# Optimization experiments

Hardware: AMD Instinct MI355X
Metric: run time of the kernel (lower is better)

The kernel has to match this reference:

```python
import jax, jax.numpy as jnp
import numpy as np

B, F, D, H, E, K = 4, 2048, 1024, 2048, 8, 2  # batch, frames, dim, expert hidden, n_experts, top_k


def setup_inputs() -> dict:
    key = jax.random.key(0)
    ks = jax.random.split(key, 9)
    sc = lambda k, shape, fan_in: (jax.random.normal(k, shape, jnp.float32) * (fan_in ** -0.5))
    return {
        "x": jax.random.normal(ks[0], (B, F, D), jnp.float32),
        # router: Linear(D,D) -> SiLU -> Linear(D,E)
        "rw1": sc(ks[1], (D, D), D),
        "rb1": jnp.zeros((D,), jnp.float32),
        "rw2": sc(ks[2], (D, E), D),
        "rb2": jnp.zeros((E,), jnp.float32),
        # experts: E x (Linear(D,H) -> SiLU -> Linear(H,D))
        "ew1": sc(ks[3], (E, D, H), D),
        "eb1": jnp.zeros((E, H), jnp.float32),
        "ew2": sc(ks[4], (E, H, D), H),
        "eb2": jnp.zeros((E, D), jnp.float32),
    }


def reference(x, rw1, rb1, rw2, rb2, ew1, eb1, ew2, eb2):
    b, f, d = x.shape
    t = x.reshape(b * f, d)                                   # [T, D]
    # router (eval mode: no topk noise)
    logits = jax.nn.silu(t @ rw1 + rb1) @ rw2 + rb2            # [T, E]
    vals, idx = jax.lax.top_k(logits, K)                       # [T, K]
    rows = jnp.arange(t.shape[0])[:, None]
    masked = jnp.full_like(logits, -jnp.inf).at[rows, idx].set(vals)
    w = jax.nn.softmax(masked, axis=1)                         # [T, E], nonzero only on top-k
    # dense per-expert FFN, then weighted combine (residual: y starts as x)
    eh = jax.nn.silu(jnp.einsum('td,edh->teh', t, ew1) + eb1[None])   # [T, E, H]
    eo = jnp.einsum('teh,ehd->ted', eh, ew2) + eb2[None]              # [T, E, D]
    y = t + jnp.einsum('te,ted->td', w, eo)
    return y.reshape(b, f, d)
```

## Files before the change

### kernel.cpp

```cpp
#include <hip/hip_runtime.h>
#include <hip/hip_bf16.h>
#include <cstdint>
#include <cstddef>

#define T_TOK 8192
#define DDIM  1024
#define HDIM  2048
#define NEXP  8
#define TOPK  2
#define KAUG  (3 * DDIM)

typedef short bf16x8 __attribute__((ext_vector_type(8)));
typedef float f32x4  __attribute__((ext_vector_type(4)));

__device__ __forceinline__ unsigned short f2bf(float f) {
  union { float f; unsigned u; } v; v.f = f;
  unsigned r = v.u + 0x7FFFu + ((v.u >> 16) & 1u);
  return (unsigned short)(r >> 16);
}
__device__ __forceinline__ float bf2f(unsigned short h) {
  union { unsigned u; float f; } v; v.u = ((unsigned)h) << 16;
  return v.f;
}
__device__ __forceinline__ float silu_fast(float v) {
  return v / (1.0f + __expf(-v));
}
__device__ __forceinline__ float silu_precise(float v) {
  return v / (1.0f + expf(-v));
}

__device__ __forceinline__ void gload16(const unsigned short* g, unsigned short* l) {
  __builtin_amdgcn_global_load_lds(
      (const __attribute__((address_space(1))) unsigned int*)g,
      (__attribute__((address_space(3))) unsigned int*)l,
      16, 0, 0);
}

__global__ void split_x_kernel(const float* __restrict__ in,
                               unsigned short* __restrict__ xaug, int n4) {
  int i = blockIdx.x * blockDim.x + threadIdx.x;
  if (i >= n4) return;
  float4 v = ((const float4*)in)[i];
  int t = i / (DDIM / 4);
  int kc = (i % (DDIM / 4)) * 4;
  float f[4] = {v.x, v.y, v.z, v.w};
  ushort4 hi, lo;
  unsigned short h[4], l[4];
#pragma unroll
  for (int j = 0; j < 4; j++) {
    h[j] = f2bf(f[j]);
    l[j] = f2bf(f[j] - bf2f(h[j]));
  }
  hi.x = h[0]; hi.y = h[1]; hi.z = h[2]; hi.w = h[3];
  lo.x = l[0]; lo.y = l[1]; lo.z = l[2]; lo.w = l[3];
  *(ushort4*)&xaug[(size_t)t * KAUG + kc] = hi;
  *(ushort4*)&xaug[(size_t)t * KAUG + DDIM + kc] = hi;
  *(ushort4*)&xaug[(size_t)t * KAUG + 2 * DDIM + kc] = lo;
}

__global__ __launch_bounds__(256) void split_w_kernel(
    const float* __restrict__ in, unsigned short* __restrict__ waug) {
  __shared__ float tile[32][33];
  int c0 = blockIdx.x * 32, r0 = blockIdx.y * 32;
  int tx = threadIdx.x & 31, ty = threadIdx.x >> 5;
#pragma unroll
  for (int i = 0; i < 32; i += 8)
    tile[ty + i][tx] = in[(size_t)(r0 + ty + i) * DDIM + (c0 + tx)];
  __syncthreads();
#pragma unroll
  for (int i = 0; i < 32; i += 8) {
    float v = tile[tx][ty + i];
    unsigned short h = f2bf(v);
    unsigned short l = f2bf(v - bf2f(h));
    int n = c0 + ty + i, k = r0 + tx;
    waug[(size_t)n * KAUG + k] = h;
    waug[(size_t)n * KAUG + DDIM + k] = l;
    waug[(size_t)n * KAUG + 2 * DDIM + k] = h;
  }
}

__global__ __launch_bounds__(256) void transpose_conv_kernel(
    const float* __restrict__ in, unsigned short* __restrict__ out, int R, int C) {
  __shared__ float tile[32][33];
  const int z = blockIdx.z;
  const float* src = in + (size_t)z * R * C;
  unsigned short* dst = out + (size_t)z * R * C;
  int c0 = blockIdx.x * 32, r0 = blockIdx.y * 32;
  int tx = threadIdx.x & 31, ty = threadIdx.x >> 5;
#pragma unroll
  for (int i = 0; i < 32; i += 8)
    tile[ty + i][tx] = src[(size_t)(r0 + ty + i) * C + (c0 + tx)];
  __syncthreads();
#pragma unroll
  for (int i = 0; i < 32; i += 8)
    dst[(size_t)(c0 + ty + i) * R + (r0 + tx)] = f2bf(tile[tx][ty + i]);
}

__global__ void zero_small_kernel(int* __restrict__ counts, int* __restrict__ cursors) {
  int i = threadIdx.x;
  if (i < NEXP) { counts[i] = 0; cursors[i] = 0; }
}

template <int EPI>
__global__ __launch_bounds__(256) void gemm_mfma(
    const unsigned short* __restrict__ Abase,
    const unsigned short* __restrict__ Btbase,
    const float* __restrict__ bias,
    float* __restrict__ outF,
    unsigned short* __restrict__ outBf,
    const int* __restrict__ toks,
    const int* __restrict__ offs, const int* __restrict__ cnts,
    int N, int KD, int Astride, int numE, int nTiles, int mCap) {
  const int id = blockIdx.x;
  const int e = id % numE;
  const int r = id / numE;
  const int n0 = (r % nTiles) * 128;
  const int mb = r / nTiles;

  int ne = T_TOK, off = 0;
  if (EPI != 0) { ne = cnts[e]; off = offs[e]; }

  const unsigned short* Bt = Btbase + (size_t)e * N * KD;
  const unsigned short* A = (EPI == 2) ? (Abase + (size_t)off * Astride) : Abase;

  __shared__ unsigned short As[2][128][32];
  __shared__ unsigned short Bs[2][128][32];

  const int tid  = threadIdx.x;
  const int lane = tid & 63, wid = tid >> 6;
  const int wm = wid >> 1, wn = wid & 1;
  const int quad = lane >> 4, l16 = lane & 15;

  const int rowS0 = tid >> 2;
  const int kc0 = (tid & 3) * 8;

  const size_t brow0 = (size_t)(n0 + rowS0) * KD;
  const size_t brow1 = brow0 + (size_t)64 * KD;
  const int nIter = KD / 32;
  const int mStride = mCap * 128;

  for (int m0 = mb * 128; m0 < ne; m0 += mStride) {
    size_t arow0, arow1;
    if (EPI == 1) {
      int p0 = m0 + rowS0, p1 = m0 + rowS0 + 64;
      int t0 = (p0 < ne) ? toks[off + p0] : 0;
      int t1 = (p1 < ne) ? toks[off + p1] : 0;
      arow0 = (size_t)t0 * Astride;
      arow1 = (size_t)t1 * Astride;
    } else if (EPI == 2) {
      arow0 = (size_t)min(m0 + rowS0, ne - 1) * Astride;
      arow1 = (size_t)min(m0 + rowS0 + 64, ne - 1) * Astride;
    } else {
      arow0 = (size_t)(m0 + rowS0) * Astride;
      arow1 = arow0 + (size_t)64 * Astride;
    }

    f32x4 zf = {0.f, 0.f, 0.f, 0.f};
    f32x4 acc[4][4];
#pragma unroll
    for (int mi = 0; mi < 4; mi++)
#pragma unroll
      for (int ni = 0; ni < 4; ni++) acc[mi][ni] = zf;

    {
      unsigned short* a0 = &As[0][0][0] + wid * 512;
      unsigned short* b0 = &Bs[0][0][0] + wid * 512;
      gload16(A + arow0 + kc0, a0);
      gload16(A + arow1 + kc0, a0 + 2048);
      gload16(Bt + brow0 + kc0, b0);
      gload16(Bt + brow1 + kc0, b0 + 2048);
    }

    for (int k = 0; k < nIter; k++) {
      const int cur = k & 1;
      if (k + 1 < nIter) {
        const int nk = (k + 1) * 32;
        unsigned short* a0 = &As[cur ^ 1][0][0] + wid * 512;
        unsigned short* b0 = &Bs[cur ^ 1][0][0] + wid * 512;
        gload16(A + arow0 + nk + kc0, a0);
        gload16(A + arow1 + nk + kc0, a0 + 2048);
        gload16(Bt + brow0 + nk + kc0, b0);
        gload16(Bt + brow1 + nk + kc0, b0 + 2048);
        __builtin_amdgcn_s_waitcnt(0x0F74);
      } else {
        __builtin_amdgcn_s_waitcnt(0x0F70);
      }
      __builtin_amdgcn_s_barrier();
      bf16x8 af[4], bfr[4];
#pragma unroll
      for (int mi = 0; mi < 4; mi++)
        af[mi] = *(const bf16x8*)&As[cur][wm * 64 + mi * 16 + l16][quad * 8];
#pragma unroll
      for (int ni = 0; ni < 4; ni++)
        bfr[ni] = *(const bf16x8*)&Bs[cur][wn * 64 + ni * 16 + l16][quad * 8];
#pragma unroll
      for (int mi = 0; mi < 4; mi++)
#pragma unroll
        for (int ni = 0; ni < 4; ni++)
          acc[mi][ni] = __builtin_amdgcn_mfma_f32_16x16x32_bf16(
              af[mi], bfr[ni], acc[mi][ni], 0, 0, 0);
      __builtin_amdgcn_s_barrier();
    }

#pragma unroll
    for (int mi = 0; mi < 4; mi++) {
      const int prow_base = wm * 64 + mi * 16 + quad * 4;
#pragma unroll
      for (int rr = 0; rr < 4; rr++) {
        const int p = m0 + prow_base + rr;
        if (EPI != 0 && p >= ne) continue;
#pragma unroll
        for (int ni = 0; ni < 4; ni++) {
          const int col = n0 + wn * 64 + ni * 16 + l16;
          float v = acc[mi][ni][rr] + bias[(size_t)e * N + col];
          if (EPI == 0) {
            outF[(size_t)p * N + col] = silu_precise(v);
          } else if (EPI == 1) {
            outBf[(size_t)(off + p) * N + col] = f2bf(silu_fast(v));
          } else {
            outBf[(size_t)(off + p) * N + col] = f2bf(v);
          }
        }
      }
    }
  }
}

__global__ __launch_bounds__(256) void router2_kernel(
    const float* __restrict__ rh, const float* __restrict__ rw2,
    const float* __restrict__ rb2, float* __restrict__ logits) {
  int t = blockIdx.x * 4 + (threadIdx.x >> 6);
  int lane = threadIdx.x & 63;
  const float* row = rh + (size_t)t * DDIM;
  float acc[NEXP];
#pragma unroll
  for (int e = 0; e < NEXP; e++) acc[e] = 0.f;
  for (int k = lane; k < DDIM; k += 64) {
    float v = row[k];
    const float* w = rw2 + (size_t)k * NEXP;
#pragma unroll
    for (int e = 0; e < NEXP; e++) acc[e] += v * w[e];
  }
#pragma unroll
  for (int e = 0; e < NEXP; e++) {
#pragma unroll
    for (int off = 32; off > 0; off >>= 1) acc[e] += __shfl_xor(acc[e], off, 64);
  }
#pragma unroll
  for (int e = 0; e < NEXP; e++)
    if (lane == e) logits[(size_t)t * NEXP + e] = acc[e] + rb2[e];
}

__global__ void topk_kernel(const float* __restrict__ logits,
                            int* __restrict__ idx2, float* __restrict__ w2arr,
                            int* __restrict__ counts) {
  int t = blockIdx.x * blockDim.x + threadIdx.x;
  if (t >= T_TOK) return;
  float l[NEXP];
#pragma unroll
  for (int e = 0; e < NEXP; e++) l[e] = logits[(size_t)t * NEXP + e];
  int i1 = 0; float v1 = l[0];
#pragma unroll
  for (int e = 1; e < NEXP; e++)
    if (l[e] > v1) { v1 = l[e]; i1 = e; }
  int i2 = -1; float v2 = -3.4e38f;
#pragma unroll
  for (int e = 0; e < NEXP; e++)
    if (e != i1 && l[e] > v2) { v2 = l[e]; i2 = e; }
  float ex = expf(v2 - v1);
  float wa = 1.f / (1.f + ex);
  float wb = ex / (1.f + ex);
  idx2[t * 2] = i1; idx2[t * 2 + 1] = i2;
  w2arr[t * 2] = wa; w2arr[t * 2 + 1] = wb;
  atomicAdd(&counts[i1], 1);
  atomicAdd(&counts[i2], 1);
}

__global__ void prefix_kernel(const int* __restrict__ counts, int* __restrict__ offs) {
  if (threadIdx.x == 0 && blockIdx.x == 0) {
    int s = 0;
    for (int e = 0; e < NEXP; e++) { offs[e] = s; s += counts[e]; }
  }
}

__global__ void scatter_kernel(const int* __restrict__ idx2,
                               const int* __restrict__ offs, int* __restrict__ cursors,
                               int* __restrict__ toks, int* __restrict__ posArr) {
  int t = blockIdx.x * blockDim.x + threadIdx.x;
  if (t >= T_TOK) return;
#pragma unroll
  for (int j = 0; j < TOPK; j++) {
    int e = idx2[t * 2 + j];
    int pos = atomicAdd(&cursors[e], 1);
    int s = offs[e] + pos;
    toks[s] = t;
    posArr[t * 2 + j] = s;
  }
}

__global__ __launch_bounds__(256) void combine_kernel(
    const float* __restrict__ x, const unsigned short* __restrict__ eo,
    const int* __restrict__ posArr, const float* __restrict__ w2arr,
    float* __restrict__ y) {
  const int t = blockIdx.x;
  const int d = threadIdx.x * 4;
  const int s0 = posArr[t * 2], s1 = posArr[t * 2 + 1];
  const float w0 = w2arr[t * 2], w1 = w2arr[t * 2 + 1];
  float4 xv = *(const float4*)&x[(size_t)t * DDIM + d];
  ushort4 a = *(const ushort4*)&eo[(size_t)s0 * DDIM + d];
  ushort4 b = *(const ushort4*)&eo[(size_t)s1 * DDIM + d];
  float4 o;
  o.x = xv.x + w0 * bf2f(a.x) + w1 * bf2f(b.x);
  o.y = xv.y + w0 * bf2f(a.y) + w1 * bf2f(b.y);
  o.z = xv.z + w0 * bf2f(a.z) + w1 * bf2f(b.z);
  o.w = xv.w + w0 * bf2f(a.w) + w1 * bf2f(b.w);
  *(float4*)&y[(size_t)t * DDIM + d] = o;
}

extern "C" void kernel_launch(void* const* d_in, const int* in_sizes, int n_in,
                              void* d_out, int out_size, void* d_ws, size_t ws_size,
                              hipStream_t stream) {
  (void)in_sizes; (void)n_in; (void)out_size; (void)ws_size;
  const float* x   = (const float*)d_in[0];
  const float* rw1 = (const float*)d_in[1];
  const float* rb1 = (const float*)d_in[2];
  const float* rw2 = (const float*)d_in[3];
  const float* rb2 = (const float*)d_in[4];
  const float* ew1 = (const float*)d_in[5];
  const float* eb1 = (const float*)d_in[6];
  const float* ew2 = (const float*)d_in[7];
  const float* eb2 = (const float*)d_in[8];
  float* y = (float*)d_out;

  char* ws = (char*)d_ws;
  size_t o = 0;
  auto alloc = [&](size_t bytes) {
    size_t r = o;
    o += (bytes + 255) & ~(size_t)255;
    return r;
  };
  unsigned short* xaug  = (unsigned short*)(ws + alloc((size_t)T_TOK * KAUG * 2));
  unsigned short* waug  = (unsigned short*)(ws + alloc((size_t)DDIM * KAUG * 2));
  unsigned short* ew1t  = (unsigned short*)(ws + alloc((size_t)NEXP * HDIM * DDIM * 2));
  unsigned short* ew2t  = (unsigned short*)(ws + alloc((size_t)NEXP * DDIM * HDIM * 2));
  float*          rh    = (float*)(ws + alloc((size_t)T_TOK * DDIM * 4));
  float*          logits= (float*)(ws + alloc((size_t)T_TOK * NEXP * 4));
  int*            idx2  = (int*)(ws + alloc((size_t)T_TOK * 2 * 4));
  float*          w2    = (float*)(ws + alloc((size_t)T_TOK * 2 * 4));
  int*            toks  = (int*)(ws + alloc((size_t)T_TOK * TOPK * 4));
  int*            posArr= (int*)(ws + alloc((size_t)T_TOK * TOPK * 4));
  int*            counts= (int*)(ws + alloc(256));
  int*            cursors=(int*)(ws + alloc(256));
  int*            offs  = (int*)(ws + alloc(256));
  unsigned short* ehb   = (unsigned short*)(ws + alloc((size_t)T_TOK * TOPK * HDIM * 2));
  unsigned short* eo    = (unsigned short*)(ws + alloc((size_t)T_TOK * TOPK * DDIM * 2));

  zero_small_kernel<<<1, 64, 0, stream>>>(counts, cursors);

  const int n4 = T_TOK * DDIM / 4;
  split_x_kernel<<<(n4 + 255) / 256, 256, 0, stream>>>(x, xaug, n4);
  split_w_kernel<<<dim3(DDIM / 32, DDIM / 32), 256, 0, stream>>>(rw1, waug);
  transpose_conv_kernel<<<dim3(HDIM / 32, DDIM / 32, NEXP), 256, 0, stream>>>(ew1, ew1t, DDIM, HDIM);
  transpose_conv_kernel<<<dim3(DDIM / 32, HDIM / 32, NEXP), 256, 0, stream>>>(ew2, ew2t, HDIM, DDIM);

  gemm_mfma<0><<<512, 256, 0, stream>>>(
      xaug, waug, rb1, rh, nullptr, nullptr, nullptr, nullptr,
      DDIM, KAUG, KAUG, 1, 8, 64);
  router2_kernel<<<T_TOK / 4, 256, 0, stream>>>(rh, rw2, rb2, logits);
  topk_kernel<<<T_TOK / 256, 256, 0, stream>>>(logits, idx2, w2, counts);
  prefix_kernel<<<1, 64, 0, stream>>>(counts, offs);
  scatter_kernel<<<T_TOK / 256, 256, 0, stream>>>(idx2, offs, cursors, toks, posArr);

  gemm_mfma<1><<<8 * 16 * 16, 256, 0, stream>>>(
      xaug, ew1t, eb1, nullptr, ehb, toks, offs, counts,
      HDIM, DDIM, KAUG, NEXP, 16, 16);
  gemm_mfma<2><<<8 * 8 * 32, 256, 0, stream>>>(
      ehb, ew2t, eb2, nullptr, eo, nullptr, offs, counts,
      DDIM, HDIM, HDIM, NEXP, 8, 32);
  combine_kernel<<<T_TOK, 256, 0, stream>>>(x, eo, posArr, w2, y);
}
```

Baseline: 806.4 us.

## Rewrite MFMA GEMM with 256-row tiles, 512 threads, swizzled LDS and split prefetch

Replaces the 128x128, 256-thread GEMM with a templated kernel that uses 256xBNT tiles, 8 waves and 64-wide K steps. Operands are staged in swizzled dynamic LDS of up to 128KB. The A and B prefetches for the next step are interleaved between two MFMA half-steps, with s_setprio raised around the MFMA blocks. The aim is more operand reuse per LDS load, fewer bank conflicts and better overlap of global loads with MFMA for the router and both expert GEMMs. The cost is much larger LDS and register use per block, which can cut occupancy, and coarser tiles that may waste work on ragged expert counts.

```diff
diff --git a/kernel.cpp b/kernel.cpp
--- a/kernel.cpp
+++ b/kernel.cpp
@@ -101,8 +101,8 @@
   if (i < NEXP) { counts[i] = 0; cursors[i] = 0; }
 }
 
-template <int EPI>
-__global__ __launch_bounds__(256) void gemm_mfma(
+template <int EPI, int BNT>
+__global__ __launch_bounds__(512, 2) void gemm_mfma2(
     const unsigned short* __restrict__ Abase,
     const unsigned short* __restrict__ Btbase,
     const float* __restrict__ bias,
@@ -111,10 +111,15 @@
     const int* __restrict__ toks,
     const int* __restrict__ offs, const int* __restrict__ cnts,
     int N, int KD, int Astride, int numE, int nTiles, int mCap) {
+  constexpr int NI = BNT / 64;
+  constexpr int RB = BNT / 64;
+  constexpr int BB = BNT * 128;
+  extern __shared__ char sm[];
+
   const int id = blockIdx.x;
   const int e = id % numE;
   const int r = id / numE;
-  const int n0 = (r % nTiles) * 128;
+  const int n0 = (r % nTiles) * BNT;
   const int mb = r / nTiles;
 
   int ne = T_TOK, off = 0;
@@ -123,96 +128,129 @@
   const unsigned short* Bt = Btbase + (size_t)e * N * KD;
   const unsigned short* A = (EPI == 2) ? (Abase + (size_t)off * Astride) : Abase;
 
-  __shared__ unsigned short As[2][128][32];
-  __shared__ unsigned short Bs[2][128][32];
-
-  const int tid  = threadIdx.x;
+  const int tid = threadIdx.x;
   const int lane = tid & 63, wid = tid >> 6;
-  const int wm = wid >> 1, wn = wid & 1;
-  const int quad = lane >> 4, l16 = lane & 15;
-
-  const int rowS0 = tid >> 2;
-  const int kc0 = (tid & 3) * 8;
-
-  const size_t brow0 = (size_t)(n0 + rowS0) * KD;
-  const size_t brow1 = brow0 + (size_t)64 * KD;
-  const int nIter = KD / 32;
-  const int mStride = mCap * 128;
-
-  for (int m0 = mb * 128; m0 < ne; m0 += mStride) {
-    size_t arow0, arow1;
-    if (EPI == 1) {
-      int p0 = m0 + rowS0, p1 = m0 + rowS0 + 64;
-      int t0 = (p0 < ne) ? toks[off + p0] : 0;
-      int t1 = (p1 < ne) ? toks[off + p1] : 0;
-      arow0 = (size_t)t0 * Astride;
-      arow1 = (size_t)t1 * Astride;
-    } else if (EPI == 2) {
-      arow0 = (size_t)min(m0 + rowS0, ne - 1) * Astride;
-      arow1 = (size_t)min(m0 + rowS0 + 64, ne - 1) * Astride;
-    } else {
-      arow0 = (size_t)(m0 + rowS0) * Astride;
-      arow1 = arow0 + (size_t)64 * Astride;
+  const int l16 = lane & 15, quad = lane >> 4;
+  const int wm = wid >> 2, wn = wid & 3;
+
+  const int rStage = tid >> 3;
+  const int cS8 = ((tid & 7) ^ (rStage & 7)) * 8;
+  const int ldsW = wid << 10;
+
+  const int NT = KD / 64;
+  const int mStride = mCap * 256;
+
+  const int sw = l16 & 7;
+  const int cOff0 = (quad ^ sw) << 4;
+  const int cOff1 = ((quad + 4) ^ sw) << 4;
+  const int aRowB = (wm * 128 + l16) << 7;
+  const int bRowB = (wn * (NI * 16) + l16) << 7;
+
+  const unsigned short* bPtr[RB];
+#pragma unroll
+  for (int p = 0; p < RB; p++)
+    bPtr[p] = Bt + (size_t)(n0 + p * 64 + rStage) * KD + cS8;
+
+  for (int m0 = mb * 256; m0 < ne; m0 += mStride) {
+    const unsigned short* aPtr[4];
+#pragma unroll
+    for (int p = 0; p < 4; p++) {
+      int row = m0 + p * 64 + rStage;
+      int idx;
+      if (EPI == 1) idx = toks[off + min(row, ne - 1)];
+      else if (EPI == 2) idx = min(row, ne - 1);
+      else idx = row;
+      aPtr[p] = A + (size_t)idx * Astride + cS8;
     }
 
-    f32x4 zf = {0.f, 0.f, 0.f, 0.f};
-    f32x4 acc[4][4];
-#pragma unroll
-    for (int mi = 0; mi < 4; mi++)
-#pragma unroll
-      for (int ni = 0; ni < 4; ni++) acc[mi][ni] = zf;
-
-    {
-      unsigned short* a0 = &As[0][0][0] + wid * 512;
-      unsigned short* b0 = &Bs[0][0][0] + wid * 512;
-      gload16(A + arow0 + kc0, a0);
-      gload16(A + arow1 + kc0, a0 + 2048);
-      gload16(Bt + brow0 + kc0, b0);
-      gload16(Bt + brow1 + kc0, b0 + 2048);
+    f32x4 acc[8][NI];
+    const f32x4 zf = {0.f, 0.f, 0.f, 0.f};
+#pragma unroll
+    for (int mi = 0; mi < 8; mi++)
+#pragma unroll
+      for (int ni = 0; ni < NI; ni++) acc[mi][ni] = zf;
+
+#pragma unroll
+    for (int p = 0; p < 4; p++)
+      gload16(aPtr[p], (unsigned short*)(sm + p * 8192 + ldsW));
+#pragma unroll
+    for (int p = 0; p < RB; p++)
+      gload16(bPtr[p], (unsigned short*)(sm + 65536 + p * 8192 + ldsW));
+    __builtin_amdgcn_s_waitcnt(0x0F70);
+    __builtin_amdgcn_s_barrier();
+    __builtin_amdgcn_sched_barrier(0);
+
+    int cur = 0;
+    for (int t = 0; t < NT; ++t) {
+      const int nxt = cur ^ 1;
+      const bool pf = (t + 1) < NT;
+      const int kb = (t + 1) * 64;
+      const char* cbA = sm + cur * 32768;
+      const char* cbB = sm + 65536 + cur * BB;
+
+      if (pf) {
+#pragma unroll
+        for (int p = 0; p < 4; p++)
+          gload16(aPtr[p] + kb, (unsigned short*)(sm + nxt * 32768 + p * 8192 + ldsW));
+      }
+      bf16x8 av[8], bv[NI];
+#pragma unroll
+      for (int mi = 0; mi < 8; mi++)
+        av[mi] = *(const bf16x8*)(cbA + aRowB + (mi << 11) + cOff0);
+#pragma unroll
+      for (int ni = 0; ni < NI; ni++)
+        bv[ni] = *(const bf16x8*)(cbB + bRowB + (ni << 11) + cOff0);
+      __builtin_amdgcn_s_barrier();
+      __builtin_amdgcn_s_setprio(1);
+#pragma unroll
+      for (int mi = 0; mi < 8; mi++)
+#pragma unroll
+        for (int ni = 0; ni < NI; ni++)
+          acc[mi][ni] = __builtin_amdgcn_mfma_f32_16x16x32_bf16(
+              av[mi], bv[ni], acc[mi][ni], 0, 0, 0);
+      __builtin_amdgcn_s_setprio(0);
+
+      if (pf) {
+#pragma unroll
+        for (int p = 0; p < RB; p++)
+          gload16(bPtr[p] + kb,
+                  (unsigned short*)(sm + 65536 + nxt * BB + p * 8192 + ldsW));
+      }
+#pragma unroll
+      for (int mi = 0; mi < 8; mi++)
+        av[mi] = *(const bf16x8*)(cbA + aRowB + (mi << 11) + cOff1);
+#pragma unroll
+      for (int ni = 0; ni < NI; ni++)
+        bv[ni] = *(const bf16x8*)(cbB + bRowB + (ni << 11) + cOff1);
+      __builtin_amdgcn_s_setprio(1);
+#pragma unroll
+      for (int mi = 0; mi < 8; mi++)
+#pragma unroll
+        for (int ni = 0; ni < NI; ni++)
+          acc[mi][ni] = __builtin_amdgcn_mfma_f32_16x16x32_bf16(
+              av[mi], bv[ni], acc[mi][ni], 0, 0, 0);
+      __builtin_amdgcn_s_setprio(0);
+      __builtin_amdgcn_s_waitcnt(0x0F70);
+      __builtin_amdgcn_s_barrier();
+      __builtin_amdgcn_sched_barrier(0);
+      cur = nxt;
     }
 
-    for (int k = 0; k < nIter; k++) {
-      const int cur = k & 1;
-      if (k + 1 < nIter) {
-        const int nk = (k + 1) * 32;
-        unsigned short* a0 = &As[cur ^ 1][0][0] + wid * 512;
-        unsigned short* b0 = &Bs[cur ^ 1][0][0] + wid * 512;
-        gload16(A + arow0 + nk + kc0, a0);
-        gload16(A + arow1 + nk + kc0, a0 + 2048);
-        gload16(Bt + brow0 + nk + kc0, b0);
-        gload16(Bt + brow1 + nk + kc0, b0 + 2048);
-        __builtin_amdgcn_s_waitcnt(0x0F74);
-      } else {
-        __builtin_amdgcn_s_waitcnt(0x0F70);
-      }
-      __builtin_amdgcn_s_barrier();
-      bf16x8 af[4], bfr[4];
-#pragma unroll
-      for (int mi = 0; mi < 4; mi++)
-        af[mi] = *(const bf16x8*)&As[cur][wm * 64 + mi * 16 + l16][quad * 8];
-#pragma unroll
-      for (int ni = 0; ni < 4; ni++)
-        bfr[ni] = *(const bf16x8*)&Bs[cur][wn * 64 + ni * 16 + l16][quad * 8];
-#pragma unroll
-      for (int mi = 0; mi < 4; mi++)
-#pragma unroll
-        for (int ni = 0; ni < 4; ni++)
-          acc[mi][ni] = __builtin_amdgcn_mfma_f32_16x16x32_bf16(
-              af[mi], bfr[ni], acc[mi][ni], 0, 0, 0);
-      __builtin_amdgcn_s_barrier();
-    }
-
-#pragma unroll
-    for (int mi = 0; mi < 4; mi++) {
-      const int prow_base = wm * 64 + mi * 16 + quad * 4;
+    float bv4[NI];
+#pragma unroll
+    for (int ni = 0; ni < NI; ni++)
+      bv4[ni] = bias[(size_t)e * N + n0 + wn * (NI * 16) + ni * 16 + l16];
+#pragma unroll
+    for (int mi = 0; mi < 8; mi++) {
+      const int prow = m0 + wm * 128 + mi * 16 + quad * 4;
 #pragma unroll
       for (int rr = 0; rr < 4; rr++) {
-        const int p = m0 + prow_base + rr;
+        const int p = prow + rr;
         if (EPI != 0 && p >= ne) continue;
 #pragma unroll
-        for (int ni = 0; ni < 4; ni++) {
-          const int col = n0 + wn * 64 + ni * 16 + l16;
-          float v = acc[mi][ni][rr] + bias[(size_t)e * N + col];
+        for (int ni = 0; ni < NI; ni++) {
+          const int col = n0 + wn * (NI * 16) + ni * 16 + l16;
+          float v = acc[mi][ni][rr] + bv4[ni];
           if (EPI == 0) {
             outF[(size_t)p * N + col] = silu_precise(v);
           } else if (EPI == 1) {
@@ -355,6 +393,19 @@
   unsigned short* ehb   = (unsigned short*)(ws + alloc((size_t)T_TOK * TOPK * HDIM * 2));
   unsigned short* eo    = (unsigned short*)(ws + alloc((size_t)T_TOK * TOPK * DDIM * 2));
 
+  constexpr int LDS_R = 98304;
+  constexpr int LDS_E = 131072;
+  static bool s_attr = false;
+  if (!s_attr) {
+    hipFuncSetAttribute((const void*)gemm_mfma2<0, 128>,
+                        hipFuncAttributeMaxDynamicSharedMemorySize, LDS_R);
+    hipFuncSetAttribute((const void*)gemm_mfma2<1, 256>,
+                        hipFuncAttributeMaxDynamicSharedMemorySize, LDS_E);
+    hipFuncSetAttribute((const void*)gemm_mfma2<2, 256>,
+                        hipFuncAttributeMaxDynamicSharedMemorySize, LDS_E);
+    s_attr = true;
+  }
+
   zero_small_kernel<<<1, 64, 0, stream>>>(counts, cursors);
 
   const int n4 = T_TOK * DDIM / 4;
@@ -363,19 +414,19 @@
   transpose_conv_kernel<<<dim3(HDIM / 32, DDIM / 32, NEXP), 256, 0, stream>>>(ew1, ew1t, DDIM, HDIM);
   transpose_conv_kernel<<<dim3(DDIM / 32, HDIM / 32, NEXP), 256, 0, stream>>>(ew2, ew2t, HDIM, DDIM);
 
-  gemm_mfma<0><<<512, 256, 0, stream>>>(
+  gemm_mfma2<0, 128><<<256, 512, LDS_R, stream>>>(
       xaug, waug, rb1, rh, nullptr, nullptr, nullptr, nullptr,
-      DDIM, KAUG, KAUG, 1, 8, 64);
+      DDIM, KAUG, KAUG, 1, 8, 32);
   router2_kernel<<<T_TOK / 4, 256, 0, stream>>>(rh, rw2, rb2, logits);
   topk_kernel<<<T_TOK / 256, 256, 0, stream>>>(logits, idx2, w2, counts);
   prefix_kernel<<<1, 64, 0, stream>>>(counts, offs);
   scatter_kernel<<<T_TOK / 256, 256, 0, stream>>>(idx2, offs, cursors, toks, posArr);
 
-  gemm_mfma<1><<<8 * 16 * 16, 256, 0, stream>>>(
+  gemm_mfma2<1, 256><<<8 * 8 * 16, 512, LDS_E, stream>>>(
       xaug, ew1t, eb1, nullptr, ehb, toks, offs, counts,
-      HDIM, DDIM, KAUG, NEXP, 16, 16);
-  gemm_mfma<2><<<8 * 8 * 32, 256, 0, stream>>>(
+      HDIM, DDIM, KAUG, NEXP, 8, 16);
+  gemm_mfma2<2, 256><<<8 * 4 * 16, 512, LDS_E, stream>>>(
       ehb, ew2t, eb2, nullptr, eo, nullptr, offs, counts,
-      DDIM, HDIM, HDIM, NEXP, 8, 32);
+      DDIM, HDIM, HDIM, NEXP, 4, 16);
   combine_kernel<<<T_TOK, 256, 0, stream>>>(x, eo, posArr, w2, y);
 }
```

Result: faster. 721.1 us (-10.6%).
